# Performance work log

Hardware: AMD Instinct MI355X
Metric: run time of the kernel (lower is better)

The kernel has to match this reference:

```python
import jax, jax.numpy as jnp
import numpy as np
import math

S, B, H, NH = 2048, 2, 2048, 16
HN = H // NH  # 128, head dim


def _rope_cache(seq_len, hn):
    # inv_freqs over even indices, half_hn entries
    inv_freqs = 0.0001 ** (jnp.arange(0, hn, 2, dtype=jnp.float32) / hn)
    pos = jnp.arange(seq_len, dtype=jnp.float32)
    angles = pos[:, None] * inv_freqs  # [s, hn/2]
    return jnp.cos(angles), jnp.sin(angles)


def _apply_rope(x, cos, sin):
    # x: [s, b, np, hn]; cos/sin: [s, hn/2] broadcast over b, np
    half = x.shape[-1] // 2
    c = cos[:, None, None, :]
    s = sin[:, None, None, :]
    left, right = x[..., :half], x[..., half:]
    return jnp.concatenate((c * left - s * right, s * left + c * right), axis=-1)


def setup_inputs() -> dict:
    key = jax.random.key(0)
    k0, k1, k2 = jax.random.split(key, 3)
    hidden_states = jax.random.normal(k0, (S, B, H), dtype=jnp.float32)
    # causal additive mask, broadcast over batch and heads
    causal = jnp.tril(jnp.ones((S, S), dtype=bool))
    attention_mask = jnp.where(causal, 0.0, -1e9).astype(jnp.float32)[None, None]
    W_qkv = jax.random.normal(k1, (3 * H, H), dtype=jnp.float32) * 0.02
    b_qkv = jnp.zeros((3 * H,), dtype=jnp.float32)
    W_dense = jax.random.normal(k2, (H, H), dtype=jnp.float32) * 0.02
    b_dense = jnp.zeros((H,), dtype=jnp.float32)
    return {"hidden_states": hidden_states, "attention_mask": attention_mask,
            "W_qkv": W_qkv, "b_qkv": b_qkv, "W_dense": W_dense, "b_dense": b_dense}


def reference(hidden_states, attention_mask, W_qkv, b_qkv, W_dense, b_dense):
    s, b, h = hidden_states.shape
    # fused QKV projection: [s,b,3h] -> [s,b,np,3*hn] -> split per head
    mixed = hidden_states @ W_qkv.T + b_qkv
    mixed = mixed.reshape(s, b, NH, 3 * HN)
    q, k, v = jnp.split(mixed, 3, axis=-1)  # each [s,b,np,hn]
    cos, sin = _rope_cache(s, HN)
    q = _apply_rope(q, cos, sin)
    k = _apply_rope(k, cos, sin)
    norm_factor = math.sqrt(HN)  # coeff is None (scale_attn_by_inverse_layer_idx=False)
    scores = jnp.einsum('sbnh,tbnh->bnst', q, k) / norm_factor  # [b,np,sq,sk]
    scores = scores + attention_mask
    probs = jax.nn.softmax(scores, axis=-1)  # dropout p=0 in eval
    ctx = jnp.einsum('bnst,tbnh->sbnh', probs, v).reshape(s, b, h)
    return ctx @ W_dense.T + b_dense  # [s,b,h]
```

## Files before the change

### kernel.cpp

```cpp
#include <hip/hip_runtime.h>

#define SEQ   2048
#define BATCH 2
#define HID   2048
#define NHEAD 16
#define HDIM  128
#define MTOT  4096
#define KDIM  2048

typedef __attribute__((ext_vector_type(8))) short  bf16x8;
typedef __attribute__((ext_vector_type(4))) float  f32x4;
typedef __attribute__((ext_vector_type(4))) unsigned short u16x4;
typedef __attribute__((ext_vector_type(8))) unsigned short u16x8;

__device__ __forceinline__ unsigned short f2bf(float x) {
  unsigned u = __float_as_uint(x);
  u += 0x7fffu + ((u >> 16) & 1u);
  return (unsigned short)(u >> 16);
}

__device__ __forceinline__ float fexp2(float x) {
  float r;
  asm("v_exp_f32 %0, %1" : "=v"(r) : "v"(x));
  return r;
}

__device__ __forceinline__ void gl_lds16(const void* g, void* l) {
  __builtin_amdgcn_global_load_lds(
      (__attribute__((address_space(1))) void*)g,
      (__attribute__((address_space(3))) void*)l, 16, 0, 0);
}

__device__ __forceinline__ f32x4 mfma16(bf16x8 a, bf16x8 b, f32x4 c) {
  return __builtin_amdgcn_mfma_f32_16x16x32_bf16(a, b, c, 0, 0, 0);
}

__global__ __launch_bounds__(256, 8)
void prep(const float* __restrict__ hidden, const float* __restrict__ Wqkv,
          const float* __restrict__ Wd,
          unsigned short* __restrict__ hidb, unsigned short* __restrict__ wqkvb,
          unsigned short* __restrict__ wdb,
          float* __restrict__ cosT, float* __restrict__ sinT) {
  int bid = blockIdx.x;
  if (bid < 24576) {
    const float* src; unsigned short* dst; int lb;
    if (bid < 8192)       { src = hidden; dst = hidb;  lb = bid; }
    else if (bid < 20480) { src = Wqkv;   dst = wqkvb; lb = bid - 8192; }
    else                  { src = Wd;     dst = wdb;   lb = bid - 20480; }
    int i = lb * 256 + threadIdx.x;
    int base = i << 2;
    int r = base >> 11, k = base & 2047;
    f32x4 v = *(const f32x4*)(src + base);
    int kp = k ^ (((r >> 1) & 3) << 3);
    u16x4 o;
    o[0] = f2bf(v[0]); o[1] = f2bf(v[1]); o[2] = f2bf(v[2]); o[3] = f2bf(v[3]);
    *(u16x4*)(dst + (size_t)r * 2048 + kp) = o;
  } else {
    int idx = (bid - 24576) * 256 + threadIdx.x;
    int s = idx >> 6, i = idx & 63;
    float inv = powf(1e-4f, (float)i * (1.0f / 64.0f));
    float a = (float)s * inv;
    cosT[idx] = cosf(a);
    sinT[idx] = sinf(a);
  }
}

__global__ __launch_bounds__(512, 2)
void gemm_qkv(const unsigned short* __restrict__ A,
              const unsigned short* __restrict__ Bt,
              const float* __restrict__ bias,
              unsigned short* __restrict__ Qs,
              unsigned short* __restrict__ Ks,
              unsigned short* __restrict__ Vt,
              const float* __restrict__ cosT,
              const float* __restrict__ sinT)
{
  __shared__ alignas(16) char lds[98304];
  const int tid = threadIdx.x;
  const int wid = tid >> 6, lane = tid & 63, g = lane >> 4, c = lane & 15;
  const int wr = wid >> 2, wc = wid & 3;

  const int bid = blockIdx.x;
  const int swz = (bid & 7) * 64 + (bid >> 3);
  const int nblk = swz & 15, mblk = swz >> 4;
  const int m0 = mblk << 7;
  const int n0 = nblk * 384;
  const int nh = nblk;

  char* ldsb = (char*)lds;
  const int slotg = (g ^ ((c >> 1) & 3)) << 4;
  const char* ldsAr = ldsb + (wr * 64 + c) * 64 + slotg;
  const char* ldsBr = ldsb + 24576 + (wc * 16 + c) * 64 + slotg;

  const char* gA = (const char*)A  + (size_t)(m0 + (tid >> 2)) * 4096 + (tid & 3) * 16;
  const char* gB = (const char*)Bt + (size_t)(n0 + (tid >> 2)) * 4096 + (tid & 3) * 16;
  char* lA = ldsb + tid * 16;
  char* lB = ldsb + 24576 + tid * 16;

#define STG_A(T, BUF) gl_lds16(gA + (T) * 64, lA + (BUF) * 8192)
#define STG_B(T, BUF) do { const char* _g = gB + (T) * 64; char* _l = lB + (BUF) * 24576; \
    gl_lds16(_g, _l); gl_lds16(_g + 524288, _l + 8192); gl_lds16(_g + 1048576, _l + 16384); } while (0)

  f32x4 acc[4][6];
#pragma unroll
  for (int i = 0; i < 4; ++i)
#pragma unroll
    for (int j = 0; j < 6; ++j) {
      acc[i][j][0] = 0.f; acc[i][j][1] = 0.f; acc[i][j][2] = 0.f; acc[i][j][3] = 0.f;
    }

  bf16x8 a[4], b[6];
  const int NT = KDIM / 32;

#define TILE(T, BUF, BUFN) do {                                             \
    if ((T) + 2 < NT) { STG_A((T) + 2, BUFN); STG_B((T) + 2, BUFN); }       \
    _Pragma("unroll")                                                       \
    for (int mf = 0; mf < 4; ++mf)                                          \
      a[mf] = *(const bf16x8*)(ldsAr + (BUF) * 8192 + mf * 1024);           \
    _Pragma("unroll")                                                       \
    for (int nl = 0; nl < 6; ++nl)                                          \
      b[nl] = *(const bf16x8*)(ldsBr + (BUF) * 24576 + nl * 4096);          \
    __builtin_amdgcn_s_setprio(1);                                          \
    _Pragma("unroll")                                                       \
    for (int mf = 0; mf < 4; ++mf)                                          \
      _Pragma("unroll")                                                     \
      for (int nl = 0; nl < 6; ++nl)                                        \
        acc[mf][nl] = mfma16(a[mf], b[nl], acc[mf][nl]);                    \
    __builtin_amdgcn_s_setprio(0);                                          \
    if ((T) + 2 < NT) { asm volatile("s_waitcnt vmcnt(4)" ::: "memory"); }  \
    else              { asm volatile("s_waitcnt vmcnt(0)" ::: "memory"); }  \
    __builtin_amdgcn_s_barrier();                                           \
  } while (0)

  STG_A(0, 0); STG_B(0, 0);
  STG_A(1, 1); STG_B(1, 1);
  asm volatile("s_waitcnt vmcnt(4)" ::: "memory");
  __builtin_amdgcn_s_barrier();

  for (int t = 0; t < 63; t += 3) {
    TILE(t, 0, 2);
    TILE(t + 1, 1, 0);
    TILE(t + 2, 2, 1);
  }
  TILE(63, 0, 2);

  const float qsc = 0.08838834764831845f * 1.4426950408889634f;
  const int dl = wc * 16 + c;
  unsigned short* Vtmp = (unsigned short*)ldsb;
  const int s0 = m0 >> 1;
#pragma unroll
  for (int ar = 0; ar < 4; ++ar) {
#pragma unroll
    for (int rr = 0; rr < 4; ++rr) {
      int m = m0 + wr * 64 + ar * 16 + g * 4 + rr;
      int s = m >> 1, bb = m & 1;
      size_t plane = (size_t)(bb * NHEAD + nh) * (SEQ * HDIM);
      int swb = (s & 7) << 3;
      float co = cosT[s * 64 + dl], si = sinT[s * 64 + dl];
      {
        float xl = acc[ar][0][rr] + bias[n0 + dl];
        float xr = acc[ar][1][rr] + bias[n0 + 64 + dl];
        Qs[plane + (size_t)s * HDIM + (dl ^ swb)]        = f2bf((co * xl - si * xr) * qsc);
        Qs[plane + (size_t)s * HDIM + ((dl + 64) ^ swb)] = f2bf((si * xl + co * xr) * qsc);
      }
      {
        float xl = acc[ar][2][rr] + bias[n0 + 128 + dl];
        float xr = acc[ar][3][rr] + bias[n0 + 192 + dl];
        Ks[plane + (size_t)s * HDIM + (dl ^ swb)]        = f2bf(co * xl - si * xr);
        Ks[plane + (size_t)s * HDIM + ((dl + 64) ^ swb)] = f2bf(si * xl + co * xr);
      }
      {
        int sloc = s - s0;
        Vtmp[(bb * 64 + sloc) * 136 + dl]      = f2bf(acc[ar][4][rr] + bias[n0 + 256 + dl]);
        Vtmp[(bb * 64 + sloc) * 136 + dl + 64] = f2bf(acc[ar][5][rr] + bias[n0 + 320 + dl]);
      }
    }
  }
  __syncthreads();
  {
    int b2 = tid >> 8, r = tid & 255;
    int d = r >> 1, half = r & 1;
    size_t planeV = (size_t)(b2 * NHEAD + nh) * (SEQ * HDIM);
    unsigned short* dstp = Vt + planeV + (size_t)d * SEQ + s0;
    int swb = (d & 7) << 3;
#pragma unroll
    for (int gg = 0; gg < 4; ++gg) {
      u16x8 v;
#pragma unroll
      for (int e = 0; e < 8; ++e)
        v[e] = Vtmp[(b2 * 64 + half * 32 + gg * 8 + e) * 136 + d];
      int tloc = half * 32 + gg * 8;
      *(u16x8*)(dstp + (tloc ^ swb)) = v;
    }
  }
#undef TILE
#undef STG_A
#undef STG_B
}

__global__ __launch_bounds__(512, 2)
void gemm_out(const unsigned short* __restrict__ A,
              const unsigned short* __restrict__ Bt,
              const float* __restrict__ bias,
              float* __restrict__ Cout)
{
  __shared__ alignas(16) char lds[73728];
  const int tid = threadIdx.x;
  const int wid = tid >> 6, lane = tid & 63, g = lane >> 4, c = lane & 15;
  const int wr = wid >> 2, wc = wid & 3;

  const int bid = blockIdx.x;
  const int swz = (bid & 7) * 32 + (bid >> 3);
  const int nblk = swz >> 5, mblk = swz & 31;
  const int m0 = mblk << 7, n0 = nblk << 8;

  char* ldsb = (char*)lds;
  const int slotg = (g ^ ((c >> 1) & 3)) << 4;
  const char* ldsAr = ldsb + (wr * 64 + c) * 64 + slotg;
  const char* ldsBr = ldsb + 24576 + (wc * 64 + c) * 64 + slotg;

  const char* gA = (const char*)A  + (size_t)(m0 + (tid >> 2)) * 4096 + (tid & 3) * 16;
  const char* gB = (const char*)Bt + (size_t)(n0 + (tid >> 2)) * 4096 + (tid & 3) * 16;
  char* lA = ldsb + tid * 16;
  char* lB = ldsb + 24576 + tid * 16;

#define STG_A(T, BUF) gl_lds16(gA + (T) * 64, lA + (BUF) * 8192)
#define STG_B(T, BUF) do { const char* _g = gB + (T) * 64; char* _l = lB + (BUF) * 16384; \
    gl_lds16(_g, _l); gl_lds16(_g + 524288, _l + 8192); } while (0)

  f32x4 acc[4][4];
#pragma unroll
  for (int i = 0; i < 4; ++i)
#pragma unroll
    for (int j = 0; j < 4; ++j) {
      acc[i][j][0] = 0.f; acc[i][j][1] = 0.f; acc[i][j][2] = 0.f; acc[i][j][3] = 0.f;
    }

  bf16x8 a[4], b[4];
  const int NT = KDIM / 32;

#define TILE(T, BUF, BUFN) do {                                             \
    if ((T) + 2 < NT) { STG_A((T) + 2, BUFN); STG_B((T) + 2, BUFN); }       \
    _Pragma("unroll")                                                       \
    for (int mf = 0; mf < 4; ++mf)                                          \
      a[mf] = *(const bf16x8*)(ldsAr + (BUF) * 8192 + mf * 1024);           \
    _Pragma("unroll")                                                       \
    for (int nl = 0; nl < 4; ++nl)                                          \
      b[nl] = *(const bf16x8*)(ldsBr + (BUF) * 16384 + nl * 1024);          \
    __builtin_amdgcn_s_setprio(1);                                          \
    _Pragma("unroll")                                                       \
    for (int mf = 0; mf < 4; ++mf)                                          \
      _Pragma("unroll")                                                     \
      for (int nl = 0; nl < 4; ++nl)                                        \
        acc[mf][nl] = mfma16(a[mf], b[nl], acc[mf][nl]);                    \
    __builtin_amdgcn_s_setprio(0);                                          \
    if ((T) + 2 < NT) { asm volatile("s_waitcnt vmcnt(3)" ::: "memory"); }  \
    else              { asm volatile("s_waitcnt vmcnt(0)" ::: "memory"); }  \
    __builtin_amdgcn_s_barrier();                                           \
  } while (0)

  STG_A(0, 0); STG_B(0, 0);
  STG_A(1, 1); STG_B(1, 1);
  asm volatile("s_waitcnt vmcnt(3)" ::: "memory");
  __builtin_amdgcn_s_barrier();

  for (int t = 0; t < 63; t += 3) {
    TILE(t, 0, 2);
    TILE(t + 1, 1, 0);
    TILE(t + 2, 2, 1);
  }
  TILE(63, 0, 2);

#pragma unroll
  for (int mf = 0; mf < 4; ++mf)
#pragma unroll
    for (int rr = 0; rr < 4; ++rr) {
      int m = m0 + wr * 64 + mf * 16 + g * 4 + rr;
#pragma unroll
      for (int nl = 0; nl < 4; ++nl) {
        int n = n0 + wc * 64 + nl * 16 + c;
        Cout[(size_t)m * HID + n] = acc[mf][nl][rr] + bias[n];
      }
    }
#undef TILE
#undef STG_A
#undef STG_B
}

__global__ __launch_bounds__(512, 2)
void attn(const unsigned short* __restrict__ Qs,
          const unsigned short* __restrict__ Ks,
          const unsigned short* __restrict__ Vt,
          unsigned short* __restrict__ ctx)
{
  __shared__ alignas(16) unsigned short Klds[2][64 * 128];
  __shared__ alignas(16) unsigned short Vlds[128 * 64];
  __shared__ alignas(16) unsigned short Plds[256 * 72];
  const int tid = threadIdx.x;
  const int w = tid >> 6, lane = tid & 63, g = lane >> 4, c = lane & 15;
  const int bid = blockIdx.x;
  const int head = bid & 31;
  const int j = bid >> 5;
  const int qbh = 15 - j;
  const int q0w = (w < 4) ? ((qbh << 7) + w * 32) : ((j << 7) + (w - 4) * 32);
  const size_t plane = (size_t)head * (SEQ * HDIM);
  const unsigned short* Qp = Qs + plane;

  bf16x8 qf[2][4];
#pragma unroll
  for (int q2 = 0; q2 < 2; ++q2) {
    int s = q0w + q2 * 16 + c;
    int swb = (s & 7) << 3;
#pragma unroll
    for (int kk = 0; kk < 4; ++kk) {
      int d0 = kk * 32 + g * 8;
      qf[q2][kk] = *(const bf16x8*)(Qp + (size_t)s * HDIM + (d0 ^ swb));
    }
  }

  f32x4 accO[2][8];
#pragma unroll
  for (int i = 0; i < 2; ++i)
#pragma unroll
    for (int jj = 0; jj < 8; ++jj) {
      accO[i][jj][0] = 0.f; accO[i][jj][1] = 0.f; accO[i][jj][2] = 0.f; accO[i][jj][3] = 0.f;
    }
  float mrun[2] = { -1e30f, -1e30f };
  float lrun[2] = { 0.f, 0.f };

  const char* Kg = (const char*)(Ks + plane) + (tid >> 4) * 256 + (tid & 15) * 16;
  const char* Vg = (const char*)(Vt + plane) + (size_t)(tid >> 3) * 4096 + (tid & 7) * 16;

  const int ntiles = (qbh << 1) + 2;
  const int qminw = q0w;
  const int qmaxw = q0w + 31;

  gl_lds16(Kg,        (char*)Klds[0] + tid * 16);
  gl_lds16(Kg + 8192, (char*)Klds[0] + tid * 16 + 8192);

  for (int kt = 0; kt < ntiles; ++kt) {
    const int t0 = kt << 6;
    const bool havenext = (kt + 1 < ntiles);

    gl_lds16(Vg + t0 * 2,          (char*)Vlds + tid * 16);
    gl_lds16(Vg + t0 * 2 + 262144, (char*)Vlds + tid * 16 + 8192);
    if (havenext) {
      char* kd = (char*)Klds[(kt + 1) & 1] + tid * 16;
      gl_lds16(Kg + (size_t)(t0 + 64) * 256,        kd);
      gl_lds16(Kg + (size_t)(t0 + 64) * 256 + 8192, kd + 8192);
    }
    if (havenext) asm volatile("s_waitcnt vmcnt(4)" ::: "memory");
    else          asm volatile("s_waitcnt vmcnt(2)" ::: "memory");
    __builtin_amdgcn_s_barrier();

    if (t0 <= qmaxw) {
      const char* Kb = (const char*)Klds[kt & 1];
      f32x4 sacc[4][2];
#pragma unroll
      for (int i = 0; i < 4; ++i)
#pragma unroll
        for (int jj = 0; jj < 2; ++jj) {
          sacc[i][jj][0] = 0.f; sacc[i][jj][1] = 0.f; sacc[i][jj][2] = 0.f; sacc[i][jj][3] = 0.f;
        }
      __builtin_amdgcn_s_setprio(1);
#pragma unroll
      for (int kk = 0; kk < 4; ++kk) {
        bf16x8 kf[4];
#pragma unroll
        for (int ta = 0; ta < 4; ++ta) {
          int t = ta * 16 + c;
          int d0 = kk * 32 + g * 8;
          kf[ta] = *(const bf16x8*)(Kb + t * 256 + ((d0 ^ ((t & 7) << 3)) << 1));
        }
#pragma unroll
        for (int ta = 0; ta < 4; ++ta)
#pragma unroll
          for (int q2 = 0; q2 < 2; ++q2)
            sacc[ta][q2] = mfma16(kf[ta], qf[q2][kk], sacc[ta][q2]);
      }
      __builtin_amdgcn_s_setprio(0);

      if (t0 + 63 > qminw) {
#pragma unroll
        for (int ta = 0; ta < 4; ++ta)
#pragma unroll
          for (int q2 = 0; q2 < 2; ++q2)
#pragma unroll
            for (int r = 0; r < 4; ++r) {
              int t = t0 + ta * 16 + g * 4 + r;
              int q = qminw + q2 * 16 + c;
              if (t > q) sacc[ta][q2][r] = -30000.f;
            }
      }

      float corr[2];
      bool resc = false;
#pragma unroll
      for (int q2 = 0; q2 < 2; ++q2) {
        float mx = -30000.f;
#pragma unroll
        for (int ta = 0; ta < 4; ++ta)
          mx = fmaxf(mx, fmaxf(fmaxf(sacc[ta][q2][0], sacc[ta][q2][1]),
                               fmaxf(sacc[ta][q2][2], sacc[ta][q2][3])));
        mx = fmaxf(mx, __shfl_xor(mx, 16));
        mx = fmaxf(mx, __shfl_xor(mx, 32));
        bool rs = mx > mrun[q2] + 8.0f;
        resc |= rs;
        float mnew = rs ? mx : mrun[q2];
        corr[q2] = fexp2(mrun[q2] - mnew);
        mrun[q2] = mnew;
        float ls = 0.f;
#pragma unroll
        for (int ta = 0; ta < 4; ++ta)
#pragma unroll
          for (int r = 0; r < 4; ++r) {
            float e = fexp2(sacc[ta][q2][r] - mnew);
            sacc[ta][q2][r] = e;
            ls += e;
          }
        ls += __shfl_xor(ls, 16);
        ls += __shfl_xor(ls, 32);
        lrun[q2] = lrun[q2] * corr[q2] + ls;
      }

      if (__any(resc)) {
#pragma unroll
        for (int q2 = 0; q2 < 2; ++q2)
#pragma unroll
          for (int r = 0; r < 4; ++r) {
            float cD = __shfl(corr[q2], (lane & 48) | (((lane >> 4) << 2) + r));
#pragma unroll
            for (int fn = 0; fn < 8; ++fn) accO[q2][fn][r] *= cD;
          }
      }

#pragma unroll
      for (int q2 = 0; q2 < 2; ++q2) {
        int prow = w * 32 + q2 * 16 + c;
#pragma unroll
        for (int ta = 0; ta < 4; ++ta) {
          u16x4 pk;
          pk[0] = f2bf(sacc[ta][q2][0]); pk[1] = f2bf(sacc[ta][q2][1]);
          pk[2] = f2bf(sacc[ta][q2][2]); pk[3] = f2bf(sacc[ta][q2][3]);
          *(u16x4*)(&Plds[prow * 72 + ta * 16 + g * 4]) = pk;
        }
      }
    }

    if (havenext) asm volatile("s_waitcnt vmcnt(2)" ::: "memory");
    else          asm volatile("s_waitcnt vmcnt(0)" ::: "memory");
    __builtin_amdgcn_s_barrier();

    if (t0 <= qmaxw) {
      __builtin_amdgcn_s_setprio(1);
#pragma unroll
      for (int kk = 0; kk < 2; ++kk) {
        bf16x8 pa[2];
#pragma unroll
        for (int q2 = 0; q2 < 2; ++q2)
          pa[q2] = *(const bf16x8*)((const char*)Plds + (w * 32 + q2 * 16 + c) * 144 + (kk * 32 + g * 8) * 2);
#pragma unroll
        for (int fn = 0; fn < 8; ++fn) {
          int d = fn * 16 + c;
          int tt = kk * 32 + g * 8;
          bf16x8 vb = *(const bf16x8*)((const char*)Vlds + d * 128 + ((tt ^ ((d & 7) << 3)) << 1));
#pragma unroll
          for (int q2 = 0; q2 < 2; ++q2)
            accO[q2][fn] = mfma16(pa[q2], vb, accO[q2][fn]);
        }
      }
      __builtin_amdgcn_s_setprio(0);
    }
    __builtin_amdgcn_s_barrier();
  }

  const int b = head >> 4, nh = head & 15;
  float linv[2] = { 1.0f / lrun[0], 1.0f / lrun[1] };
#pragma unroll
  for (int q2 = 0; q2 < 2; ++q2)
#pragma unroll
    for (int r = 0; r < 4; ++r) {
      float inv = __shfl(linv[q2], (lane & 48) | (((lane >> 4) << 2) + r));
      int q = q0w + q2 * 16 + g * 4 + r;
      int m = q * 2 + b;
      int swb = ((m >> 1) & 3) << 3;
#pragma unroll
      for (int fn = 0; fn < 8; ++fn) {
        int h = nh * 128 + fn * 16 + c;
        ctx[(size_t)m * HID + (h ^ swb)] = f2bf(accO[q2][fn][r] * inv);
      }
    }
}

extern "C" void kernel_launch(void* const* d_in, const int* in_sizes, int n_in,
                              void* d_out, int out_size, void* d_ws, size_t ws_size,
                              hipStream_t stream) {
  const float* hidden = (const float*)d_in[0];
  const float* Wqkv = (const float*)d_in[2];
  const float* bqkv = (const float*)d_in[3];
  const float* Wd   = (const float*)d_in[4];
  const float* bd   = (const float*)d_in[5];
  float* out = (float*)d_out;
  char* ws = (char*)d_ws;

  const size_t OFF_HID  = 0;
  const size_t OFF_WQKV = 16777216;
  const size_t OFF_WD   = 41943040;
  const size_t OFF_COS  = 50331648;
  const size_t OFF_SIN  = 50855936;
  const size_t OFF_Q    = 51380224;
  const size_t OFF_K    = 68157440;
  const size_t OFF_VT   = 84934656;
  if (ws_size < 101711872) return;

  unsigned short* hidb  = (unsigned short*)(ws + OFF_HID);
  unsigned short* wqkvb = (unsigned short*)(ws + OFF_WQKV);
  unsigned short* wdb   = (unsigned short*)(ws + OFF_WD);
  float* cosT = (float*)(ws + OFF_COS);
  float* sinT = (float*)(ws + OFF_SIN);
  unsigned short* Qsb = (unsigned short*)(ws + OFF_Q);
  unsigned short* Ksb = (unsigned short*)(ws + OFF_K);
  unsigned short* Vtb = (unsigned short*)(ws + OFF_VT);
  unsigned short* ctxb = hidb;

  prep<<<25088, 256, 0, stream>>>(hidden, Wqkv, Wd, hidb, wqkvb, wdb, cosT, sinT);

  gemm_qkv<<<512, 512, 0, stream>>>(hidb, wqkvb, bqkv, Qsb, Ksb, Vtb, cosT, sinT);
  attn<<<256, 512, 0, stream>>>(Qsb, Ksb, Vtb, ctxb);
  gemm_out<<<256, 512, 0, stream>>>(ctxb, wdb, bd, out);
}
```

Baseline: 242.6 us.

## Double GEMM K-tile to 64 with asymmetric A/B LDS buffering and 8-way swizzle

Both GEMM kernels now stage 64-wide K tiles instead of 32, halving the number of barrier-synchronised iterations, and the pre-swizzle in prep and attn's ctx write widens from 4 to 8 slots to match 128-byte LDS rows. The QKV GEMM triple-buffers A but only double-buffers the large B tile to stay within LDS, and reorders prefetch distances to match. The output GEMM keeps a triple buffer of both. LDS use rises to 144KB per block, which limits blocks per CU and may reduce occupancy and latency hiding.

```diff
diff --git a/kernel.cpp b/kernel.cpp
--- a/kernel.cpp
+++ b/kernel.cpp
@@ -51,7 +51,7 @@
     int base = i << 2;
     int r = base >> 11, k = base & 2047;
     f32x4 v = *(const f32x4*)(src + base);
-    int kp = k ^ (((r >> 1) & 3) << 3);
+    int kp = k ^ (((r >> 1) & 7) << 3);
     u16x4 o;
     o[0] = f2bf(v[0]); o[1] = f2bf(v[1]); o[2] = f2bf(v[2]); o[3] = f2bf(v[3]);
     *(u16x4*)(dst + (size_t)r * 2048 + kp) = o;
@@ -75,7 +75,7 @@
               const float* __restrict__ cosT,
               const float* __restrict__ sinT)
 {
-  __shared__ alignas(16) char lds[98304];
+  __shared__ alignas(16) char lds[147456];
   const int tid = threadIdx.x;
   const int wid = tid >> 6, lane = tid & 63, g = lane >> 4, c = lane & 15;
   const int wr = wid >> 2, wc = wid & 3;
@@ -88,18 +88,23 @@
   const int nh = nblk;
 
   char* ldsb = (char*)lds;
-  const int slotg = (g ^ ((c >> 1) & 3)) << 4;
-  const char* ldsAr = ldsb + (wr * 64 + c) * 64 + slotg;
-  const char* ldsBr = ldsb + 24576 + (wc * 16 + c) * 64 + slotg;
-
-  const char* gA = (const char*)A  + (size_t)(m0 + (tid >> 2)) * 4096 + (tid & 3) * 16;
-  const char* gB = (const char*)Bt + (size_t)(n0 + (tid >> 2)) * 4096 + (tid & 3) * 16;
+  const int sw = c >> 1;
+  const char* ldsA0 = ldsb + (wr * 64 + c) * 128 + ((g ^ sw) << 4);
+  const char* ldsA1 = ldsb + (wr * 64 + c) * 128 + (((4 + g) ^ sw) << 4);
+  const char* ldsB0 = ldsb + 49152 + (wc * 16 + c) * 128 + ((g ^ sw) << 4);
+  const char* ldsB1 = ldsb + 49152 + (wc * 16 + c) * 128 + (((4 + g) ^ sw) << 4);
+
+  const char* gA = (const char*)A  + (size_t)(m0 + (tid >> 3)) * 4096 + (tid & 7) * 16;
+  const char* gB = (const char*)Bt + (size_t)(n0 + (tid >> 3)) * 4096 + (tid & 7) * 16;
   char* lA = ldsb + tid * 16;
-  char* lB = ldsb + 24576 + tid * 16;
-
-#define STG_A(T, BUF) gl_lds16(gA + (T) * 64, lA + (BUF) * 8192)
-#define STG_B(T, BUF) do { const char* _g = gB + (T) * 64; char* _l = lB + (BUF) * 24576; \
-    gl_lds16(_g, _l); gl_lds16(_g + 524288, _l + 8192); gl_lds16(_g + 1048576, _l + 16384); } while (0)
+  char* lB = ldsb + 49152 + tid * 16;
+
+#define STG_A(T, BUF) do { const char* _g = gA + (T) * 128; char* _l = lA + (BUF) * 16384; \
+    gl_lds16(_g, _l); gl_lds16(_g + 262144, _l + 8192); } while (0)
+#define STG_B(T, BUF) do { const char* _g = gB + (T) * 128; char* _l = lB + (BUF) * 49152; \
+    gl_lds16(_g, _l);           gl_lds16(_g + 262144, _l + 8192);   \
+    gl_lds16(_g + 524288, _l + 16384); gl_lds16(_g + 786432, _l + 24576); \
+    gl_lds16(_g + 1048576, _l + 32768); gl_lds16(_g + 1310720, _l + 40960); } while (0)
 
   f32x4 acc[4][6];
 #pragma unroll
@@ -110,16 +115,15 @@
     }
 
   bf16x8 a[4], b[6];
-  const int NT = KDIM / 32;
-
-#define TILE(T, BUF, BUFN) do {                                             \
-    if ((T) + 2 < NT) { STG_A((T) + 2, BUFN); STG_B((T) + 2, BUFN); }       \
+  const int NT = KDIM / 64;
+
+#define HALF(PA, PB, SA, SB) do {                                           \
     _Pragma("unroll")                                                       \
     for (int mf = 0; mf < 4; ++mf)                                          \
-      a[mf] = *(const bf16x8*)(ldsAr + (BUF) * 8192 + mf * 1024);           \
+      a[mf] = *(const bf16x8*)(PA + (SA) * 16384 + mf * 2048);              \
     _Pragma("unroll")                                                       \
     for (int nl = 0; nl < 6; ++nl)                                          \
-      b[nl] = *(const bf16x8*)(ldsBr + (BUF) * 24576 + nl * 4096);          \
+      b[nl] = *(const bf16x8*)(PB + (SB) * 49152 + nl * 8192);              \
     __builtin_amdgcn_s_setprio(1);                                          \
     _Pragma("unroll")                                                       \
     for (int mf = 0; mf < 4; ++mf)                                          \
@@ -127,22 +131,32 @@
       for (int nl = 0; nl < 6; ++nl)                                        \
         acc[mf][nl] = mfma16(a[mf], b[nl], acc[mf][nl]);                    \
     __builtin_amdgcn_s_setprio(0);                                          \
-    if ((T) + 2 < NT) { asm volatile("s_waitcnt vmcnt(4)" ::: "memory"); }  \
+  } while (0)
+
+#define TILE(T, SA, SB) do {                                                \
+    if ((T) + 1 < NT) { STG_B((T) + 1, ((T) + 1) & 1); }                    \
+    if ((T) + 2 < NT) { STG_A((T) + 2, ((T) + 2) % 3); }                    \
+    HALF(ldsA0, ldsB0, SA, SB);                                             \
+    HALF(ldsA1, ldsB1, SA, SB);                                             \
+    if ((T) + 2 < NT) { asm volatile("s_waitcnt vmcnt(2)" ::: "memory"); }  \
     else              { asm volatile("s_waitcnt vmcnt(0)" ::: "memory"); }  \
     __builtin_amdgcn_s_barrier();                                           \
   } while (0)
 
-  STG_A(0, 0); STG_B(0, 0);
-  STG_A(1, 1); STG_B(1, 1);
-  asm volatile("s_waitcnt vmcnt(4)" ::: "memory");
+  STG_B(0, 0); STG_A(0, 0); STG_A(1, 1);
+  asm volatile("s_waitcnt vmcnt(2)" ::: "memory");
   __builtin_amdgcn_s_barrier();
 
-  for (int t = 0; t < 63; t += 3) {
-    TILE(t, 0, 2);
-    TILE(t + 1, 1, 0);
-    TILE(t + 2, 2, 1);
-  }
-  TILE(63, 0, 2);
+  for (int t = 0; t < 30; t += 6) {
+    TILE(t + 0, 0, 0);
+    TILE(t + 1, 1, 1);
+    TILE(t + 2, 2, 0);
+    TILE(t + 3, 0, 1);
+    TILE(t + 4, 1, 0);
+    TILE(t + 5, 2, 1);
+  }
+  TILE(30, 0, 0);
+  TILE(31, 1, 1);
 
   const float qsc = 0.08838834764831845f * 1.4426950408889634f;
   const int dl = wc * 16 + c;
@@ -194,6 +208,7 @@
     }
   }
 #undef TILE
+#undef HALF
 #undef STG_A
 #undef STG_B
 }
@@ -204,7 +219,7 @@
               const float* __restrict__ bias,
               float* __restrict__ Cout)
 {
-  __shared__ alignas(16) char lds[73728];
+  __shared__ alignas(16) char lds[147456];
   const int tid = threadIdx.x;
   const int wid = tid >> 6, lane = tid & 63, g = lane >> 4, c = lane & 15;
   const int wr = wid >> 2, wc = wid & 3;
@@ -215,18 +230,22 @@
   const int m0 = mblk << 7, n0 = nblk << 8;
 
   char* ldsb = (char*)lds;
-  const int slotg = (g ^ ((c >> 1) & 3)) << 4;
-  const char* ldsAr = ldsb + (wr * 64 + c) * 64 + slotg;
-  const char* ldsBr = ldsb + 24576 + (wc * 64 + c) * 64 + slotg;
-
-  const char* gA = (const char*)A  + (size_t)(m0 + (tid >> 2)) * 4096 + (tid & 3) * 16;
-  const char* gB = (const char*)Bt + (size_t)(n0 + (tid >> 2)) * 4096 + (tid & 3) * 16;
+  const int sw = c >> 1;
+  const char* ldsA0 = ldsb + (wr * 64 + c) * 128 + ((g ^ sw) << 4);
+  const char* ldsA1 = ldsb + (wr * 64 + c) * 128 + (((4 + g) ^ sw) << 4);
+  const char* ldsB0 = ldsb + 49152 + (wc * 64 + c) * 128 + ((g ^ sw) << 4);
+  const char* ldsB1 = ldsb + 49152 + (wc * 64 + c) * 128 + (((4 + g) ^ sw) << 4);
+
+  const char* gA = (const char*)A  + (size_t)(m0 + (tid >> 3)) * 4096 + (tid & 7) * 16;
+  const char* gB = (const char*)Bt + (size_t)(n0 + (tid >> 3)) * 4096 + (tid & 7) * 16;
   char* lA = ldsb + tid * 16;
-  char* lB = ldsb + 24576 + tid * 16;
-
-#define STG_A(T, BUF) gl_lds16(gA + (T) * 64, lA + (BUF) * 8192)
-#define STG_B(T, BUF) do { const char* _g = gB + (T) * 64; char* _l = lB + (BUF) * 16384; \
-    gl_lds16(_g, _l); gl_lds16(_g + 524288, _l + 8192); } while (0)
+  char* lB = ldsb + 49152 + tid * 16;
+
+#define STG_A(T, BUF) do { const char* _g = gA + (T) * 128; char* _l = lA + (BUF) * 16384; \
+    gl_lds16(_g, _l); gl_lds16(_g + 262144, _l + 8192); } while (0)
+#define STG_B(T, BUF) do { const char* _g = gB + (T) * 128; char* _l = lB + (BUF) * 32768; \
+    gl_lds16(_g, _l);           gl_lds16(_g + 262144, _l + 8192);   \
+    gl_lds16(_g + 524288, _l + 16384); gl_lds16(_g + 786432, _l + 24576); } while (0)
 
   f32x4 acc[4][4];
 #pragma unroll
@@ -237,16 +256,15 @@
     }
 
   bf16x8 a[4], b[4];
-  const int NT = KDIM / 32;
-
-#define TILE(T, BUF, BUFN) do {                                             \
-    if ((T) + 2 < NT) { STG_A((T) + 2, BUFN); STG_B((T) + 2, BUFN); }       \
+  const int NT = KDIM / 64;
+
+#define HALF(PA, PB, S) do {                                                \
     _Pragma("unroll")                                                       \
     for (int mf = 0; mf < 4; ++mf)                                          \
-      a[mf] = *(const bf16x8*)(ldsAr + (BUF) * 8192 + mf * 1024);           \
+      a[mf] = *(const bf16x8*)(PA + (S) * 16384 + mf * 2048);               \
     _Pragma("unroll")                                                       \
     for (int nl = 0; nl < 4; ++nl)                                          \
-      b[nl] = *(const bf16x8*)(ldsBr + (BUF) * 16384 + nl * 1024);          \
+      b[nl] = *(const bf16x8*)(PB + (S) * 32768 + nl * 2048);               \
     __builtin_amdgcn_s_setprio(1);                                          \
     _Pragma("unroll")                                                       \
     for (int mf = 0; mf < 4; ++mf)                                          \
@@ -254,22 +272,29 @@
       for (int nl = 0; nl < 4; ++nl)                                        \
         acc[mf][nl] = mfma16(a[mf], b[nl], acc[mf][nl]);                    \
     __builtin_amdgcn_s_setprio(0);                                          \
-    if ((T) + 2 < NT) { asm volatile("s_waitcnt vmcnt(3)" ::: "memory"); }  \
+  } while (0)
+
+#define TILE(T, S) do {                                                     \
+    if ((T) + 2 < NT) { STG_B((T) + 2, ((T) + 2) % 3); STG_A((T) + 2, ((T) + 2) % 3); } \
+    HALF(ldsA0, ldsB0, S);                                                  \
+    HALF(ldsA1, ldsB1, S);                                                  \
+    if ((T) + 2 < NT) { asm volatile("s_waitcnt vmcnt(6)" ::: "memory"); }  \
     else              { asm volatile("s_waitcnt vmcnt(0)" ::: "memory"); }  \
     __builtin_amdgcn_s_barrier();                                           \
   } while (0)
 
-  STG_A(0, 0); STG_B(0, 0);
-  STG_A(1, 1); STG_B(1, 1);
-  asm volatile("s_waitcnt vmcnt(3)" ::: "memory");
+  STG_B(0, 0); STG_A(0, 0);
+  STG_B(1, 1); STG_A(1, 1);
+  asm volatile("s_waitcnt vmcnt(6)" ::: "memory");
   __builtin_amdgcn_s_barrier();
 
-  for (int t = 0; t < 63; t += 3) {
-    TILE(t, 0, 2);
-    TILE(t + 1, 1, 0);
-    TILE(t + 2, 2, 1);
-  }
-  TILE(63, 0, 2);
+  for (int t = 0; t < 30; t += 3) {
+    TILE(t, 0);
+    TILE(t + 1, 1);
+    TILE(t + 2, 2);
+  }
+  TILE(30, 0);
+  TILE(31, 1);
 
 #pragma unroll
   for (int mf = 0; mf < 4; ++mf)
@@ -283,6 +308,7 @@
       }
     }
 #undef TILE
+#undef HALF
 #undef STG_A
 #undef STG_B
 }
@@ -483,7 +509,7 @@
       float inv = __shfl(linv[q2], (lane & 48) | (((lane >> 4) << 2) + r));
       int q = q0w + q2 * 16 + g * 4 + r;
       int m = q * 2 + b;
-      int swb = ((m >> 1) & 3) << 3;
+      int swb = ((m >> 1) & 7) << 3;
 #pragma unroll
       for (int fn = 0; fn < 8; ++fn) {
         int h = nh * 128 + fn * 16 + c;
```

Result: faster. 231.3 us (-4.7%).

## Shrink GEMM LDS footprint and tiles to raise occupancy for QKV and output GEMMs

Applied to the files above, without the earlier changes.

The QKV GEMM moves from a uniform triple buffer to a triple-buffered A tile and a double-buffered B tile. This shrinks LDS from 96KB to 72KB, and launch bounds are raised to allow more blocks per CU. The output GEMM halves its N tile to 128 and doubles the grid to 512 blocks, cutting LDS to 48KB to fill more CUs and raise occupancy. The cost is less prefetch depth for B in the QKV GEMM and less reuse per block in the output GEMM, which could expose memory latency.

```diff
diff --git a/kernel.cpp b/kernel.cpp
--- a/kernel.cpp
+++ b/kernel.cpp
@@ -65,7 +65,7 @@
   }
 }
 
-__global__ __launch_bounds__(512, 2)
+__global__ __launch_bounds__(512, 4)
 void gemm_qkv(const unsigned short* __restrict__ A,
               const unsigned short* __restrict__ Bt,
               const float* __restrict__ bias,
@@ -75,7 +75,7 @@
               const float* __restrict__ cosT,
               const float* __restrict__ sinT)
 {
-  __shared__ alignas(16) char lds[98304];
+  __shared__ alignas(16) char lds[73728];
   const int tid = threadIdx.x;
   const int wid = tid >> 6, lane = tid & 63, g = lane >> 4, c = lane & 15;
   const int wr = wid >> 2, wc = wid & 3;
@@ -112,14 +112,15 @@
   bf16x8 a[4], b[6];
   const int NT = KDIM / 32;
 
-#define TILE(T, BUF, BUFN) do {                                             \
-    if ((T) + 2 < NT) { STG_A((T) + 2, BUFN); STG_B((T) + 2, BUFN); }       \
+#define TILE(T, SA, SB) do {                                                \
+    if ((T) + 1 < NT) { STG_B((T) + 1, ((T) + 1) & 1); }                    \
+    if ((T) + 2 < NT) { STG_A((T) + 2, ((T) + 2) % 3); }                    \
     _Pragma("unroll")                                                       \
     for (int mf = 0; mf < 4; ++mf)                                          \
-      a[mf] = *(const bf16x8*)(ldsAr + (BUF) * 8192 + mf * 1024);           \
+      a[mf] = *(const bf16x8*)(ldsAr + (SA) * 8192 + mf * 1024);            \
     _Pragma("unroll")                                                       \
     for (int nl = 0; nl < 6; ++nl)                                          \
-      b[nl] = *(const bf16x8*)(ldsBr + (BUF) * 24576 + nl * 4096);          \
+      b[nl] = *(const bf16x8*)(ldsBr + (SB) * 24576 + nl * 4096);           \
     __builtin_amdgcn_s_setprio(1);                                          \
     _Pragma("unroll")                                                       \
     for (int mf = 0; mf < 4; ++mf)                                          \
@@ -127,22 +128,27 @@
       for (int nl = 0; nl < 6; ++nl)                                        \
         acc[mf][nl] = mfma16(a[mf], b[nl], acc[mf][nl]);                    \
     __builtin_amdgcn_s_setprio(0);                                          \
-    if ((T) + 2 < NT) { asm volatile("s_waitcnt vmcnt(4)" ::: "memory"); }  \
+    if ((T) + 2 < NT) { asm volatile("s_waitcnt vmcnt(1)" ::: "memory"); }  \
     else              { asm volatile("s_waitcnt vmcnt(0)" ::: "memory"); }  \
     __builtin_amdgcn_s_barrier();                                           \
   } while (0)
 
-  STG_A(0, 0); STG_B(0, 0);
-  STG_A(1, 1); STG_B(1, 1);
-  asm volatile("s_waitcnt vmcnt(4)" ::: "memory");
+  STG_B(0, 0); STG_A(0, 0); STG_A(1, 1);
+  asm volatile("s_waitcnt vmcnt(1)" ::: "memory");
   __builtin_amdgcn_s_barrier();
 
-  for (int t = 0; t < 63; t += 3) {
-    TILE(t, 0, 2);
-    TILE(t + 1, 1, 0);
-    TILE(t + 2, 2, 1);
-  }
-  TILE(63, 0, 2);
+  for (int t = 0; t < 60; t += 6) {
+    TILE(t + 0, 0, 0);
+    TILE(t + 1, 1, 1);
+    TILE(t + 2, 2, 0);
+    TILE(t + 3, 0, 1);
+    TILE(t + 4, 1, 0);
+    TILE(t + 5, 2, 1);
+  }
+  TILE(60, 0, 0);
+  TILE(61, 1, 1);
+  TILE(62, 2, 0);
+  TILE(63, 0, 1);
 
   const float qsc = 0.08838834764831845f * 1.4426950408889634f;
   const int dl = wc * 16 + c;
@@ -198,26 +204,26 @@
 #undef STG_B
 }
 
-__global__ __launch_bounds__(512, 2)
+__global__ __launch_bounds__(512, 4)
 void gemm_out(const unsigned short* __restrict__ A,
               const unsigned short* __restrict__ Bt,
               const float* __restrict__ bias,
               float* __restrict__ Cout)
 {
-  __shared__ alignas(16) char lds[73728];
+  __shared__ alignas(16) char lds[49152];
   const int tid = threadIdx.x;
   const int wid = tid >> 6, lane = tid & 63, g = lane >> 4, c = lane & 15;
   const int wr = wid >> 2, wc = wid & 3;
 
   const int bid = blockIdx.x;
-  const int swz = (bid & 7) * 32 + (bid >> 3);
-  const int nblk = swz >> 5, mblk = swz & 31;
-  const int m0 = mblk << 7, n0 = nblk << 8;
+  const int swz = (bid & 7) * 64 + (bid >> 3);
+  const int nblk = swz & 15, mblk = swz >> 4;
+  const int m0 = mblk << 7, n0 = nblk << 7;
 
   char* ldsb = (char*)lds;
   const int slotg = (g ^ ((c >> 1) & 3)) << 4;
   const char* ldsAr = ldsb + (wr * 64 + c) * 64 + slotg;
-  const char* ldsBr = ldsb + 24576 + (wc * 64 + c) * 64 + slotg;
+  const char* ldsBr = ldsb + 24576 + (wc * 32 + c) * 64 + slotg;
 
   const char* gA = (const char*)A  + (size_t)(m0 + (tid >> 2)) * 4096 + (tid & 3) * 16;
   const char* gB = (const char*)Bt + (size_t)(n0 + (tid >> 2)) * 4096 + (tid & 3) * 16;
@@ -225,51 +231,50 @@
   char* lB = ldsb + 24576 + tid * 16;
 
 #define STG_A(T, BUF) gl_lds16(gA + (T) * 64, lA + (BUF) * 8192)
-#define STG_B(T, BUF) do { const char* _g = gB + (T) * 64; char* _l = lB + (BUF) * 16384; \
-    gl_lds16(_g, _l); gl_lds16(_g + 524288, _l + 8192); } while (0)
-
-  f32x4 acc[4][4];
+#define STG_B(T, BUF) gl_lds16(gB + (T) * 64, lB + (BUF) * 8192)
+
+  f32x4 acc[4][2];
 #pragma unroll
   for (int i = 0; i < 4; ++i)
 #pragma unroll
-    for (int j = 0; j < 4; ++j) {
+    for (int j = 0; j < 2; ++j) {
       acc[i][j][0] = 0.f; acc[i][j][1] = 0.f; acc[i][j][2] = 0.f; acc[i][j][3] = 0.f;
     }
 
-  bf16x8 a[4], b[4];
+  bf16x8 a[4], b[2];
   const int NT = KDIM / 32;
 
-#define TILE(T, BUF, BUFN) do {                                             \
-    if ((T) + 2 < NT) { STG_A((T) + 2, BUFN); STG_B((T) + 2, BUFN); }       \
+#define TILE(T, S) do {                                                     \
+    if ((T) + 2 < NT) { STG_B((T) + 2, ((T) + 2) % 3); STG_A((T) + 2, ((T) + 2) % 3); } \
     _Pragma("unroll")                                                       \
     for (int mf = 0; mf < 4; ++mf)                                          \
-      a[mf] = *(const bf16x8*)(ldsAr + (BUF) * 8192 + mf * 1024);           \
+      a[mf] = *(const bf16x8*)(ldsAr + (S) * 8192 + mf * 1024);             \
     _Pragma("unroll")                                                       \
-    for (int nl = 0; nl < 4; ++nl)                                          \
-      b[nl] = *(const bf16x8*)(ldsBr + (BUF) * 16384 + nl * 1024);          \
+    for (int nl = 0; nl < 2; ++nl)                                          \
+      b[nl] = *(const bf16x8*)(ldsBr + (S) * 8192 + nl * 1024);             \
     __builtin_amdgcn_s_setprio(1);                                          \
     _Pragma("unroll")                                                       \
     for (int mf = 0; mf < 4; ++mf)                                          \
       _Pragma("unroll")                                                     \
-      for (int nl = 0; nl < 4; ++nl)                                        \
+      for (int nl = 0; nl < 2; ++nl)                                        \
         acc[mf][nl] = mfma16(a[mf], b[nl], acc[mf][nl]);                    \
     __builtin_amdgcn_s_setprio(0);                                          \
-    if ((T) + 2 < NT) { asm volatile("s_waitcnt vmcnt(3)" ::: "memory"); }  \
+    if ((T) + 2 < NT) { asm volatile("s_waitcnt vmcnt(2)" ::: "memory"); }  \
     else              { asm volatile("s_waitcnt vmcnt(0)" ::: "memory"); }  \
     __builtin_amdgcn_s_barrier();                                           \
   } while (0)
 
-  STG_A(0, 0); STG_B(0, 0);
-  STG_A(1, 1); STG_B(1, 1);
-  asm volatile("s_waitcnt vmcnt(3)" ::: "memory");
+  STG_B(0, 0); STG_A(0, 0);
+  STG_B(1, 1); STG_A(1, 1);
+  asm volatile("s_waitcnt vmcnt(2)" ::: "memory");
   __builtin_amdgcn_s_barrier();
 
   for (int t = 0; t < 63; t += 3) {
-    TILE(t, 0, 2);
-    TILE(t + 1, 1, 0);
-    TILE(t + 2, 2, 1);
-  }
-  TILE(63, 0, 2);
+    TILE(t, 0);
+    TILE(t + 1, 1);
+    TILE(t + 2, 2);
+  }
+  TILE(63, 0);
 
 #pragma unroll
   for (int mf = 0; mf < 4; ++mf)
@@ -277,8 +282,8 @@
     for (int rr = 0; rr < 4; ++rr) {
       int m = m0 + wr * 64 + mf * 16 + g * 4 + rr;
 #pragma unroll
-      for (int nl = 0; nl < 4; ++nl) {
-        int n = n0 + wc * 64 + nl * 16 + c;
+      for (int nl = 0; nl < 2; ++nl) {
+        int n = n0 + wc * 32 + nl * 16 + c;
         Cout[(size_t)m * HID + n] = acc[mf][nl][rr] + bias[n];
       }
     }
@@ -527,5 +532,5 @@
 
   gemm_qkv<<<512, 512, 0, stream>>>(hidb, wqkvb, bqkv, Qsb, Ksb, Vtb, cosT, sinT);
   attn<<<256, 512, 0, stream>>>(Qsb, Ksb, Vtb, ctxb);
-  gemm_out<<<256, 512, 0, stream>>>(ctxb, wdb, bd, out);
-}
+  gemm_out<<<512, 512, 0, stream>>>(ctxb, wdb, bd, out);
+}
```

Result: slower. 547.3 us (+125.6%).
